# Optimization experiments

Hardware: AMD Instinct MI355X
Metric: run time of the kernel (lower is better)

The kernel has to match this reference:

```python
import jax, jax.numpy as jnp
import numpy as np

N_NODES = 50000
N_EDGES = 1600000
DIM_IN = 128
DIM_OUT = 128
EPS = 1e-10


def setup_inputs() -> dict:
    key = jax.random.key(0)
    k1, k2, k3, k4, k5 = jax.random.split(key, 5)
    feat_in = jax.random.normal(k1, (N_NODES, DIM_IN), dtype=jnp.float32)
    rows = jax.random.randint(k2, (N_EDGES,), 0, N_NODES, dtype=jnp.int32)
    cols = jax.random.randint(k3, (N_EDGES,), 0, N_NODES, dtype=jnp.int32)
    # normalized adjacency values (positive, ~1/deg scale)
    vals = jax.random.uniform(k4, (N_EDGES,), dtype=jnp.float32) / 32.0
    W = jax.random.normal(k5, (DIM_OUT, DIM_IN), dtype=jnp.float32) * 0.05
    b = jnp.zeros((DIM_OUT,), dtype=jnp.float32)
    scale = jnp.ones((DIM_OUT,), dtype=jnp.float32)
    offset = jnp.zeros((DIM_OUT,), dtype=jnp.float32)
    return {"feat_in": feat_in, "rows": rows, "cols": cols, "vals": vals,
            "W": W, "b": b, "scale": scale, "offset": offset}


def reference(feat_in, rows, cols, vals, W, b, scale, offset):
    # torch.sparse.mm(adj_norm, feat_in): gather source features, scale by
    # edge value, scatter-add into destination rows.
    msgs = vals[:, None] * feat_in[cols]                       # [E, D_in]
    feat_aggr = jax.ops.segment_sum(msgs, rows, num_segments=N_NODES)  # [N, D_in]
    # f_lin (nn.Linear): x @ W.T + b
    feat_trans = feat_aggr @ W.T + b                           # [N, D_out]
    # act = ReLU
    a = jax.nn.relu(feat_trans)
    # f_norm: per-row (feature-dim) normalization, biased variance
    mean = jnp.mean(a, axis=1, keepdims=True)
    var = jnp.mean((a - mean) ** 2, axis=1, keepdims=True) + EPS
    feat_out = (a - mean) * scale * jax.lax.rsqrt(var) + offset
    return feat_out
```

## Files before the change

kernel.cpp:

```cpp
#include <hip/hip_runtime.h>

typedef unsigned int uint;
typedef unsigned short ushort;
typedef __attribute__((ext_vector_type(8))) short short8;
typedef __attribute__((ext_vector_type(4))) float floatx4;

#define N_NODES 50000
#define N_EDGES 1600000
#define DIM 128
#define LN_EPS 1e-10f

#define ROWS_PER_BUCKET 64
#define N_BUCKETS 782
#define BUCKET_CAP 2560
#define SB 512
#define EPB 3125
#define CONVB 512
#define CAPR 76

__device__ __forceinline__ uint f2bf(float x) {
    uint u = __float_as_uint(x);
    return (u + 0x7FFFu + ((u >> 16) & 1u)) >> 16;
}

__global__ __launch_bounds__(512) void scatter(
    const float* __restrict__ feat, const float* __restrict__ W,
    const int* __restrict__ rows, const int* __restrict__ cols,
    const float* __restrict__ vals, int* __restrict__ gcnt,
    int2* __restrict__ perm, uint* __restrict__ featb_u,
    ushort* __restrict__ wbf)
{
    __shared__ int  cnt[N_BUCKETS];
    __shared__ int  gbase[N_BUCKETS];
    __shared__ int  lbase[N_BUCKETS];
    __shared__ int  csum[64];
    __shared__ uint stash[EPB];
    __shared__ int2 stageE[EPB];
    const int bx = blockIdx.x;
    const int t  = threadIdx.x;

    if (bx >= SB) {
        const int cb = bx - SB;
        const int stride = CONVB * 512;
        for (int i = cb * 512 + t; i < N_NODES * DIM / 4; i += stride) {
            float4 v = ((const float4*)feat)[i];
            ((uint2*)featb_u)[i] = make_uint2(
                f2bf(v.x) | (f2bf(v.y) << 16),
                f2bf(v.z) | (f2bf(v.w) << 16));
        }
        for (int i = cb * 512 + t; i < DIM * DIM / 4; i += stride) {
            float4 v = ((const float4*)W)[i];
            ushort4 o;
            o.x = (ushort)f2bf(v.x); o.y = (ushort)f2bf(v.y);
            o.z = (ushort)f2bf(v.z); o.w = (ushort)f2bf(v.w);
            ((ushort4*)wbf)[i] = o;
        }
        return;
    }

    for (int i = t; i < N_BUCKETS; i += 512) cnt[i] = 0;
    __syncthreads();
    const int base = bx * EPB;
    for (int k = t; k < EPB; k += 512) {
        int r = rows[base + k];
        int rank = atomicAdd(&cnt[r >> 6], 1);
        stash[k] = ((uint)rank << 16) | (uint)r;
    }
    __syncthreads();

    for (int i = t; i < N_BUCKETS; i += 512) {
        int c = cnt[i];
        gbase[i] = c ? atomicAdd(&gcnt[i], c) : 0;
    }
    if (t < 64) {
        int s = 0;
        for (int j = 0; j < 13; ++j) {
            int idx = t * 13 + j;
            if (idx < N_BUCKETS) s += cnt[idx];
        }
        csum[t] = s;
    }
    __syncthreads();
    if (t == 0) {
        int s = 0;
        for (int i = 0; i < 64; ++i) { int c = csum[i]; csum[i] = s; s += c; }
    }
    __syncthreads();
    if (t < 64) {
        int run = csum[t];
        for (int j = 0; j < 13; ++j) {
            int idx = t * 13 + j;
            if (idx < N_BUCKETS) { lbase[idx] = run; run += cnt[idx]; }
        }
    }
    __syncthreads();

    for (int k = t; k < EPB; k += 512) {
        int e = base + k;
        uint s = stash[k];
        int r = (int)(s & 0xFFFFu);
        int rank = (int)(s >> 16);
        int b = r >> 6;
        int pos = lbase[b] + rank;
        stageE[pos] = make_int2(
            (uint)cols[e] | ((uint)(r & 63) << 16) | ((uint)b << 22),
            __float_as_int(vals[e]));
    }
    __syncthreads();

    for (int j = t; j < EPB; j += 512) {
        int2 p = stageE[j];
        uint b = ((uint)p.x) >> 22;
        int pos = gbase[b] + (j - lbase[b]);
        if (pos < BUCKET_CAP)
            perm[(size_t)b * BUCKET_CAP + pos] = p;
    }
}

__global__ __launch_bounds__(512, 6) void agg_fused(
    const int2* __restrict__ perm, const int* __restrict__ gcnt,
    const ushort* __restrict__ featb, const ushort* __restrict__ wbf,
    const float* __restrict__ bias, const float* __restrict__ scale,
    const float* __restrict__ offset, float* __restrict__ out)
{
    __shared__ int2 lists[32 * CAPR];
    ushort* rowsbuf = (ushort*)lists;
    float*  Cbuf    = (float*)lists;
    __shared__ int  lcnt[32];

    const int t = threadIdx.x;

    const int nwg = N_BUCKETS * 2;
    const int q = nwg >> 3, rr = nwg & 7;
    const int xcd = blockIdx.x & 7, within = blockIdx.x >> 3;
    const int w = (xcd < rr ? xcd * (q + 1) : rr * (q + 1) + (xcd - rr) * q) + within;
    const int b  = w >> 1;
    const int lo = (w & 1) * 32;

    if (t < 32) lcnt[t] = 0;
    __syncthreads();

    int n = gcnt[b];
    if (n > BUCKET_CAP) n = BUCKET_CAP;
    const int2* pb = perm + (size_t)b * BUCKET_CAP;

    for (int e = t; e < n; e += 512) {
        int2 p = pb[e];
        int rl = ((p.x >> 16) & 63) - lo;
        if ((uint)rl < 32u) {
            int pos = atomicAdd(&lcnt[rl], 1);
            if (pos < CAPR)
                lists[rl * CAPR + pos] = make_int2((p.x & 0xFFFF) << 8, p.y);
        }
    }
    __syncthreads();

    const int lane = t & 63;
    const int wid  = t >> 6;
    const int rb   = wid * 4;
    const char* fbase = (const char*)featb;
    const uint  lane4 = (uint)lane << 2;

    float ax[4], ay[4];
    #pragma unroll
    for (int j = 0; j < 4; ++j) {
        int rl = rb + j;
        int cnt = lcnt[rl];
        if (cnt > CAPR) cnt = CAPR;
        const int2* L = &lists[rl * CAPR];
        float sx = 0.f, sy = 0.f;
        int e = 0;
        for (; e + 7 < cnt; e += 8) {
            int2 p[8]; uint g[8];
            #pragma unroll
            for (int k = 0; k < 8; ++k) p[k] = L[e + k];
            #pragma unroll
            for (int k = 0; k < 8; ++k)
                g[k] = *(const uint*)(fbase + ((uint)p[k].x + lane4));
            #pragma unroll
            for (int k = 0; k < 8; ++k) {
                float v = __int_as_float(p[k].y);
                sx = fmaf(v, __uint_as_float(g[k] << 16), sx);
                sy = fmaf(v, __uint_as_float(g[k] & 0xFFFF0000u), sy);
            }
        }
        for (; e < cnt; ++e) {
            int2 p = L[e];
            uint g = *(const uint*)(fbase + ((uint)p.x + lane4));
            float v = __int_as_float(p.y);
            sx = fmaf(v, __uint_as_float(g << 16), sx);
            sy = fmaf(v, __uint_as_float(g & 0xFFFF0000u), sy);
        }
        ax[j] = sx; ay[j] = sy;
    }
    __syncthreads();

    #pragma unroll
    for (int j = 0; j < 4; ++j) {
        uint pk = f2bf(ax[j]) | (f2bf(ay[j]) << 16);
        *(uint*)&rowsbuf[(rb + j) * 136 + 2 * lane] = pk;
    }
    __syncthreads();

    const int l15  = lane & 15;
    const int quad = lane >> 4;
    const int n0   = wid * 16 + l15;
    const float bb = bias[n0];

    floatx4 acc0 = {0.f, 0.f, 0.f, 0.f};
    floatx4 acc1 = {0.f, 0.f, 0.f, 0.f};
    #pragma unroll
    for (int kt = 0; kt < 4; ++kt) {
        int k0 = kt * 32 + quad * 8;
        short8 af0 = *(const short8*)&rowsbuf[l15 * 136 + k0];
        short8 af1 = *(const short8*)&rowsbuf[(l15 + 16) * 136 + k0];
        short8 bf  = *(const short8*)&wbf[n0 * DIM + k0];
        acc0 = __builtin_amdgcn_mfma_f32_16x16x32_bf16(af0, bf, acc0, 0, 0, 0);
        acc1 = __builtin_amdgcn_mfma_f32_16x16x32_bf16(af1, bf, acc1, 0, 0, 0);
    }
    __syncthreads();

    #pragma unroll
    for (int r = 0; r < 4; ++r) {
        int m = quad * 4 + r;
        Cbuf[m * 132 + n0]        = acc0[r] + bb;
        Cbuf[(m + 16) * 132 + n0] = acc1[r] + bb;
    }
    __syncthreads();

    const float sc0 = scale[lane],  sc1 = scale[lane + 64];
    const float of0 = offset[lane], of1 = offset[lane + 64];

    #pragma unroll
    for (int j = 0; j < 4; ++j) {
        int rl = rb + j;
        int r  = b * ROWS_PER_BUCKET + lo + rl;
        if (r >= N_NODES) continue;
        float A0 = fmaxf(Cbuf[rl * 132 + lane],      0.0f);
        float A1 = fmaxf(Cbuf[rl * 132 + lane + 64], 0.0f);

        float s = A0 + A1;
        #pragma unroll
        for (int off = 32; off >= 1; off >>= 1) s += __shfl_xor(s, off, 64);
        float mean = s * (1.0f / 128.0f);

        float d0 = A0 - mean, d1 = A1 - mean;
        float q2 = d0 * d0 + d1 * d1;
        #pragma unroll
        for (int off = 32; off >= 1; off >>= 1) q2 += __shfl_xor(q2, off, 64);
        float rstd = rsqrtf(q2 * (1.0f / 128.0f) + LN_EPS);

        size_t rowp = (size_t)r * DIM;
        out[rowp + lane]      = d0 * sc0 * rstd + of0;
        out[rowp + lane + 64] = d1 * sc1 * rstd + of1;
    }
}

extern "C" void kernel_launch(void* const* d_in, const int* in_sizes, int n_in,
                              void* d_out, int out_size, void* d_ws, size_t ws_size,
                              hipStream_t stream) {
    const float* feat_in = (const float*)d_in[0];
    const int*   rows    = (const int*)d_in[1];
    const int*   cols    = (const int*)d_in[2];
    const float* vals    = (const float*)d_in[3];
    const float* W       = (const float*)d_in[4];
    const float* bias    = (const float*)d_in[5];
    const float* scale   = (const float*)d_in[6];
    const float* offset  = (const float*)d_in[7];
    float* out = (float*)d_out;

    char* p = (char*)d_ws;
    int2* perm = (int2*)p;                 p += (size_t)N_BUCKETS * BUCKET_CAP * 8;
    ushort* featb = (ushort*)p;            p += (size_t)N_NODES * DIM * 2;
    ushort* wbf = (ushort*)p;              p += DIM * DIM * 2;
    int*  gcnt = (int*)p;                  p += (size_t)(N_BUCKETS + 64) * 4;

    hipMemsetAsync(gcnt, 0, (size_t)N_BUCKETS * sizeof(int), stream);

    scatter<<<SB + CONVB, 512, 0, stream>>>(feat_in, W, rows, cols, vals,
                                            gcnt, perm, (uint*)featb, wbf);
    agg_fused<<<N_BUCKETS * 2, 512, 0, stream>>>(perm, gcnt, featb, wbf,
                                                 bias, scale, offset, out);
}
```

Measured before the change: 181.8 us.

## Use 1024-thread blocks, drop LDS staging in scatter, one bucket per block

The scatter kernel now runs 1024-thread blocks over twice as many edges each. It keeps per-edge ranks and rows in registers and writes perm entries straight to global memory, dropping the LDS prefix-sum and staging pass. The aggregation kernel processes a whole 64-row bucket per 1024-thread block, so each perm bucket is read once instead of twice, and the XCD block remapping is removed. Scattered global writes are less coalesced, and larger blocks with more LDS may lower occupancy.

```diff
diff --git a/kernel.cpp b/kernel.cpp
--- a/kernel.cpp
+++ b/kernel.cpp
@@ -13,9 +13,9 @@
 #define ROWS_PER_BUCKET 64
 #define N_BUCKETS 782
 #define BUCKET_CAP 2560
-#define SB 512
-#define EPB 3125
-#define CONVB 512
+#define SB 256
+#define EPB 6250
+#define CONVB 256
 #define CAPR 76
 
 __device__ __forceinline__ uint f2bf(float x) {
@@ -23,32 +23,27 @@
     return (u + 0x7FFFu + ((u >> 16) & 1u)) >> 16;
 }
 
-__global__ __launch_bounds__(512) void scatter(
+__global__ __launch_bounds__(1024) void scatter(
     const float* __restrict__ feat, const float* __restrict__ W,
     const int* __restrict__ rows, const int* __restrict__ cols,
     const float* __restrict__ vals, int* __restrict__ gcnt,
     int2* __restrict__ perm, uint* __restrict__ featb_u,
     ushort* __restrict__ wbf)
 {
-    __shared__ int  cnt[N_BUCKETS];
-    __shared__ int  gbase[N_BUCKETS];
-    __shared__ int  lbase[N_BUCKETS];
-    __shared__ int  csum[64];
-    __shared__ uint stash[EPB];
-    __shared__ int2 stageE[EPB];
+    __shared__ int cnt[N_BUCKETS];
+    __shared__ int gbase[N_BUCKETS];
     const int bx = blockIdx.x;
     const int t  = threadIdx.x;
 
-    if (bx >= SB) {
-        const int cb = bx - SB;
-        const int stride = CONVB * 512;
-        for (int i = cb * 512 + t; i < N_NODES * DIM / 4; i += stride) {
+    if (bx < CONVB) {
+        const int stride = CONVB * 1024;
+        for (int i = bx * 1024 + t; i < N_NODES * DIM / 4; i += stride) {
             float4 v = ((const float4*)feat)[i];
             ((uint2*)featb_u)[i] = make_uint2(
                 f2bf(v.x) | (f2bf(v.y) << 16),
                 f2bf(v.z) | (f2bf(v.w) << 16));
         }
-        for (int i = cb * 512 + t; i < DIM * DIM / 4; i += stride) {
+        for (int i = bx * 1024 + t; i < DIM * DIM / 4; i += stride) {
             float4 v = ((const float4*)W)[i];
             ushort4 o;
             o.x = (ushort)f2bf(v.x); o.y = (ushort)f2bf(v.y);
@@ -57,101 +52,70 @@
         }
         return;
     }
-
-    for (int i = t; i < N_BUCKETS; i += 512) cnt[i] = 0;
-    __syncthreads();
-    const int base = bx * EPB;
-    for (int k = t; k < EPB; k += 512) {
-        int r = rows[base + k];
-        int rank = atomicAdd(&cnt[r >> 6], 1);
-        stash[k] = ((uint)rank << 16) | (uint)r;
-    }
-    __syncthreads();
-
-    for (int i = t; i < N_BUCKETS; i += 512) {
+    const int sb   = bx - CONVB;
+    const int base = sb * EPB;
+
+    for (int i = t; i < N_BUCKETS; i += 1024) cnt[i] = 0;
+    __syncthreads();
+    int rankv[7], rowv[7];
+    #pragma unroll
+    for (int i = 0; i < 7; ++i) {
+        int k = i * 1024 + t;
+        if (k < EPB) {
+            int r = rows[base + k];
+            rowv[i]  = r;
+            rankv[i] = atomicAdd(&cnt[r >> 6], 1);
+        }
+    }
+    __syncthreads();
+
+    for (int i = t; i < N_BUCKETS; i += 1024) {
         int c = cnt[i];
         gbase[i] = c ? atomicAdd(&gcnt[i], c) : 0;
     }
-    if (t < 64) {
-        int s = 0;
-        for (int j = 0; j < 13; ++j) {
-            int idx = t * 13 + j;
-            if (idx < N_BUCKETS) s += cnt[idx];
-        }
-        csum[t] = s;
-    }
-    __syncthreads();
-    if (t == 0) {
-        int s = 0;
-        for (int i = 0; i < 64; ++i) { int c = csum[i]; csum[i] = s; s += c; }
-    }
-    __syncthreads();
-    if (t < 64) {
-        int run = csum[t];
-        for (int j = 0; j < 13; ++j) {
-            int idx = t * 13 + j;
-            if (idx < N_BUCKETS) { lbase[idx] = run; run += cnt[idx]; }
-        }
-    }
-    __syncthreads();
-
-    for (int k = t; k < EPB; k += 512) {
-        int e = base + k;
-        uint s = stash[k];
-        int r = (int)(s & 0xFFFFu);
-        int rank = (int)(s >> 16);
-        int b = r >> 6;
-        int pos = lbase[b] + rank;
-        stageE[pos] = make_int2(
-            (uint)cols[e] | ((uint)(r & 63) << 16) | ((uint)b << 22),
-            __float_as_int(vals[e]));
-    }
-    __syncthreads();
-
-    for (int j = t; j < EPB; j += 512) {
-        int2 p = stageE[j];
-        uint b = ((uint)p.x) >> 22;
-        int pos = gbase[b] + (j - lbase[b]);
-        if (pos < BUCKET_CAP)
-            perm[(size_t)b * BUCKET_CAP + pos] = p;
-    }
-}
-
-__global__ __launch_bounds__(512, 6) void agg_fused(
+    __syncthreads();
+
+    #pragma unroll
+    for (int i = 0; i < 7; ++i) {
+        int k = i * 1024 + t;
+        if (k < EPB) {
+            int r = rowv[i], b = r >> 6;
+            int pos = gbase[b] + rankv[i];
+            if (pos < BUCKET_CAP)
+                perm[(size_t)b * BUCKET_CAP + pos] = make_int2(
+                    (uint)cols[base + k] | ((uint)(r & 63) << 16),
+                    __float_as_int(vals[base + k]));
+        }
+    }
+}
+
+__global__ __launch_bounds__(1024, 8) void agg_fused(
     const int2* __restrict__ perm, const int* __restrict__ gcnt,
     const ushort* __restrict__ featb, const ushort* __restrict__ wbf,
     const float* __restrict__ bias, const float* __restrict__ scale,
     const float* __restrict__ offset, float* __restrict__ out)
 {
-    __shared__ int2 lists[32 * CAPR];
+    __shared__ int2 lists[64 * CAPR];
     ushort* rowsbuf = (ushort*)lists;
     float*  Cbuf    = (float*)lists;
-    __shared__ int  lcnt[32];
+    __shared__ int  lcnt[64];
 
     const int t = threadIdx.x;
-
-    const int nwg = N_BUCKETS * 2;
-    const int q = nwg >> 3, rr = nwg & 7;
-    const int xcd = blockIdx.x & 7, within = blockIdx.x >> 3;
-    const int w = (xcd < rr ? xcd * (q + 1) : rr * (q + 1) + (xcd - rr) * q) + within;
-    const int b  = w >> 1;
-    const int lo = (w & 1) * 32;
-
-    if (t < 32) lcnt[t] = 0;
+    const int b = blockIdx.x;
+
+    if (t < 64) lcnt[t] = 0;
     __syncthreads();
 
     int n = gcnt[b];
     if (n > BUCKET_CAP) n = BUCKET_CAP;
     const int2* pb = perm + (size_t)b * BUCKET_CAP;
 
-    for (int e = t; e < n; e += 512) {
+    for (int e = t; e < n; e += 1024) {
         int2 p = pb[e];
-        int rl = ((p.x >> 16) & 63) - lo;
-        if ((uint)rl < 32u) {
-            int pos = atomicAdd(&lcnt[rl], 1);
-            if (pos < CAPR)
-                lists[rl * CAPR + pos] = make_int2((p.x & 0xFFFF) << 8, p.y);
-        }
+        int rl = (p.x >> 16) & 63;
+        int pos = atomicAdd(&lcnt[rl], 1);
+        if (pos < CAPR)
+            lists[rl * CAPR + pos] = make_int2((p.x & 0xFFFF) << 8, p.y);
     }
     __syncthreads();
 
@@ -204,7 +168,8 @@
 
     const int l15  = lane & 15;
     const int quad = lane >> 4;
-    const int n0   = wid * 16 + l15;
+    const int n0   = (wid & 7) * 16 + l15;
+    const int m0   = (wid >> 3) * 32;
     const float bb = bias[n0];
 
     floatx4 acc0 = {0.f, 0.f, 0.f, 0.f};
@@ -212,8 +177,8 @@
     #pragma unroll
     for (int kt = 0; kt < 4; ++kt) {
         int k0 = kt * 32 + quad * 8;
-        short8 af0 = *(const short8*)&rowsbuf[l15 * 136 + k0];
-        short8 af1 = *(const short8*)&rowsbuf[(l15 + 16) * 136 + k0];
+        short8 af0 = *(const short8*)&rowsbuf[(m0 + l15) * 136 + k0];
+        short8 af1 = *(const short8*)&rowsbuf[(m0 + l15 + 16) * 136 + k0];
         short8 bf  = *(const short8*)&wbf[n0 * DIM + k0];
         acc0 = __builtin_amdgcn_mfma_f32_16x16x32_bf16(af0, bf, acc0, 0, 0, 0);
         acc1 = __builtin_amdgcn_mfma_f32_16x16x32_bf16(af1, bf, acc1, 0, 0, 0);
@@ -222,7 +187,7 @@
 
     #pragma unroll
     for (int r = 0; r < 4; ++r) {
-        int m = quad * 4 + r;
+        int m = m0 + quad * 4 + r;
         Cbuf[m * 132 + n0]        = acc0[r] + bb;
         Cbuf[(m + 16) * 132 + n0] = acc1[r] + bb;
     }
@@ -234,7 +199,7 @@
     #pragma unroll
     for (int j = 0; j < 4; ++j) {
         int rl = rb + j;
-        int r  = b * ROWS_PER_BUCKET + lo + rl;
+        int r  = b * ROWS_PER_BUCKET + rl;
         if (r >= N_NODES) continue;
         float A0 = fmaxf(Cbuf[rl * 132 + lane],      0.0f);
         float A1 = fmaxf(Cbuf[rl * 132 + lane + 64], 0.0f);
@@ -277,8 +242,8 @@
 
     hipMemsetAsync(gcnt, 0, (size_t)N_BUCKETS * sizeof(int), stream);
 
-    scatter<<<SB + CONVB, 512, 0, stream>>>(feat_in, W, rows, cols, vals,
-                                            gcnt, perm, (uint*)featb, wbf);
-    agg_fused<<<N_BUCKETS * 2, 512, 0, stream>>>(perm, gcnt, featb, wbf,
-                                                 bias, scale, offset, out);
-}
+    scatter<<<CONVB + SB, 1024, 0, stream>>>(feat_in, W, rows, cols, vals,
+                                             gcnt, perm, (uint*)featb, wbf);
+    agg_fused<<<N_BUCKETS, 1024, 0, stream>>>(perm, gcnt, featb, wbf,
+                                              bias, scale, offset, out);
+}
```

Measured after the change: 190.6 us. 1.05x slower.
